# Performance work log

Hardware: AMD Instinct MI355X
Metric: run time of the kernel (lower is better)

The kernel has to match this reference:

```python
import jax, jax.numpy as jnp
import numpy as np

BATCH, SEQ, H, P, N, L = 8, 8192, 16, 64, 64, 64  # batch, seq, heads, d_head, d_state, block_len


def setup_inputs() -> dict:
    key = jax.random.key(0)
    k1, k2, k3 = jax.random.split(key, 3)
    X = jax.random.normal(k1, (BATCH, SEQ, H, P), dtype=jnp.float32)
    # A is the log-decay; scale down so exp(cumsum) stays finite over 8192 steps
    A = jax.random.normal(k2, (BATCH, SEQ, H), dtype=jnp.float32) * 0.02
    B = jax.random.normal(k3, (BATCH, SEQ, H, N), dtype=jnp.float32)
    return {"X": X, "A": A, "B": B}


def reference(X, A, B):
    b, s, h, p = X.shape
    n = B.shape[-1]
    l = L
    c = s // l  # n_chunks

    Xb = X.reshape(b, c, l, h, p)                      # (b,c,l,h,p)
    Ab = A.reshape(b, c, l, h).transpose(0, 3, 1, 2)   # (b,h,c,l)
    Bb = B.reshape(b, c, l, h, n)                      # (b,c,l,h,n)

    # intra-chunk cumulative decay
    A_cs = jnp.cumsum(Ab, axis=-1)                     # (b,h,c,l)
    decay_states = jnp.exp(A_cs[..., -1:] - A_cs)      # (b,h,c,l)

    # per-chunk state: sum_l decay * B outer X -> (b,c,h,p,n)
    states = jnp.einsum('bhcl,bclhn,bclhp->bchpn', decay_states, Bb, Xb)

    # prepend zero initial state
    init = jnp.zeros((b, 1, h, p, n), dtype=X.dtype)
    all_states = jnp.concatenate([init, states], axis=1)  # (b,c+1,h,p,n)

    # cross-chunk decay-weighted combination into final state
    A_ends = A_cs[..., -1]                                # (b,h,c)
    A_pad_cs = jnp.cumsum(jnp.pad(A_ends, ((0, 0), (0, 0), (1, 0))), axis=-1)  # (b,h,c+1)
    decay_chunk = jnp.exp(A_pad_cs[..., -1:] - A_pad_cs)  # (b,h,c+1)

    final_states = jnp.einsum('bhc,bchpn->bhpn', decay_chunk, all_states)  # (b,h,p,n)
    return final_states
```

## Files before the change

### kernel.cpp

```cpp
#include <hip/hip_runtime.h>

#define BATCH 8
#define SEQ   8192
#define NH    16
#define DP    64
#define ROWF  (NH*DP)
#define HGRP  4
#define NTHR  512
#define KT    32
#define RS    260

typedef __attribute__((ext_vector_type(8))) short bf16x8;
typedef __attribute__((ext_vector_type(4))) float f32x4;

static __device__ __forceinline__ unsigned pk2(float lo, float hi) {
    unsigned a = __builtin_bit_cast(unsigned, lo);
    unsigned b = __builtin_bit_cast(unsigned, hi);
    a = (a + 0x7FFFu + ((a >> 16) & 1u)) >> 16;
    b = (b + 0x7FFFu + ((b >> 16) & 1u)) & 0xFFFF0000u;
    return (a & 0xFFFFu) | b;
}

template<int NBLK>
__global__ __launch_bounds__(NTHR)
void k_partial(const float* __restrict__ Xg, const float* __restrict__ Ag,
               const float* __restrict__ Bg, float* __restrict__ part,
               float* __restrict__ blockA)
{
    constexpr int TB  = SEQ / NBLK;
    constexpr int Q   = TB / 64;
    constexpr int NKT = TB / KT;

    __shared__ unsigned XL[16][RS];
    __shared__ unsigned BL[16][RS];
    __shared__ float    WT[HGRP][TB];

    const int p    = blockIdx.x;
    const int xcd  = p & 7;
    const int q_   = p >> 3;
    const int hg   = q_ & 3;
    const int sidx = q_ >> 2;
    const int idx  = sidx * 8 + xcd;
    const int blk  = idx % NBLK;
    const int b    = idx / NBLK;

    const int tid  = threadIdx.x;
    const int w    = tid >> 6;
    const int lane = tid & 63;
    const int hloc = w >> 1;
    const int nh   = w & 1;
    const int h    = hg * HGRP + hloc;
    const int t0   = blk * TB;

    float c[Q];
    {
        const size_t abase = ((size_t)(b * SEQ + t0 + lane * Q)) * NH + h;
        float run = 0.f;
        #pragma unroll
        for (int k = 0; k < Q; ++k) { run += Ag[abase + (size_t)k * NH]; c[k] = run; }
    }
    float tsum = c[Q - 1], s = tsum;
    #pragma unroll
    for (int d = 1; d < 64; d <<= 1) {
        float o = __shfl_up(s, d, 64);
        if (lane >= d) s += o;
    }
    const float total = __shfl(s, 63, 64);
    const float excl  = s - tsum;
    if (nh == 0) {
        #pragma unroll
        for (int k = 0; k < Q; ++k)
            WT[hloc][lane * Q + k] = __expf(total - (excl + c[k]));
        if (lane == 63) blockA[(size_t)(b * NH + h) * NBLK + blk] = total;
    }

    f32x4 acc[4][2];
    #pragma unroll
    for (int mi = 0; mi < 4; ++mi)
        #pragma unroll
        for (int ni = 0; ni < 2; ++ni) acc[mi][ni] = (f32x4){0.f, 0.f, 0.f, 0.f};

    const int hl = lane >> 4;
    const int p4 = (lane & 15) * 4;
    const size_t gbase = (size_t)(b * SEQ + t0) * ROWF + hg * (HGRP * DP) + hl * DP + p4;

    auto issue = [&](int k, float4* lx, float4* lb) {
        if (k >= NKT) return;
        const size_t tb = gbase + (size_t)(k * KT + w * 4) * ROWF;
        #pragma unroll
        for (int i = 0; i < 4; ++i) {
            lx[i] = *(const float4*)(Xg + tb + (size_t)i * ROWF);
            lb[i] = *(const float4*)(Bg + tb + (size_t)i * ROWF);
        }
    };
    auto cwrite = [&](int k, const float4* lx, const float4* lb) {
        const int tIn = k * KT + w * 4;
        #pragma unroll
        for (int q2 = 0; q2 < 2; ++q2) {
            const float w0 = WT[hl][tIn + 2 * q2];
            const float w1 = WT[hl][tIn + 2 * q2 + 1];
            const int   tp = w * 2 + q2;
            const float* x0 = (const float*)&lx[2 * q2];
            const float* x1 = (const float*)&lx[2 * q2 + 1];
            const float* b0 = (const float*)&lb[2 * q2];
            const float* b1 = (const float*)&lb[2 * q2 + 1];
            uint4 xv, bv;
            xv.x = pk2(x0[0] * w0, x1[0] * w1);
            xv.y = pk2(x0[1] * w0, x1[1] * w1);
            xv.z = pk2(x0[2] * w0, x1[2] * w1);
            xv.w = pk2(x0[3] * w0, x1[3] * w1);
            bv.x = pk2(b0[0], b1[0]);
            bv.y = pk2(b0[1], b1[1]);
            bv.z = pk2(b0[2], b1[2]);
            bv.w = pk2(b0[3], b1[3]);
            *(uint4*)&XL[tp][hl * 64 + p4] = xv;
            *(uint4*)&BL[tp][hl * 64 + p4] = bv;
        }
    };
    auto compute = [&]() {
        const int r  = lane & 15;
        const int kg = lane >> 4;
        uint4 af[4], bf[2];
        #pragma unroll
        for (int mi = 0; mi < 4; ++mi) {
            const int row = hloc * 64 + mi * 16 + r;
            af[mi].x = XL[kg * 4 + 0][row];
            af[mi].y = XL[kg * 4 + 1][row];
            af[mi].z = XL[kg * 4 + 2][row];
            af[mi].w = XL[kg * 4 + 3][row];
        }
        #pragma unroll
        for (int ni = 0; ni < 2; ++ni) {
            const int row = hloc * 64 + nh * 32 + ni * 16 + r;
            bf[ni].x = BL[kg * 4 + 0][row];
            bf[ni].y = BL[kg * 4 + 1][row];
            bf[ni].z = BL[kg * 4 + 2][row];
            bf[ni].w = BL[kg * 4 + 3][row];
        }
        #pragma unroll
        for (int mi = 0; mi < 4; ++mi) {
            const bf16x8 a = __builtin_bit_cast(bf16x8, af[mi]);
            #pragma unroll
            for (int ni = 0; ni < 2; ++ni) {
                const bf16x8 bb = __builtin_bit_cast(bf16x8, bf[ni]);
                acc[mi][ni] = __builtin_amdgcn_mfma_f32_16x16x32_bf16(
                                  a, bb, acc[mi][ni], 0, 0, 0);
            }
        }
    };

    float4 sx0[4], sb0[4], sx1[4], sb1[4];
    issue(0, sx0, sb0);
    issue(1, sx1, sb1);
    __syncthreads();

    #pragma unroll 1
    for (int k = 0; k < NKT; k += 2) {
        cwrite(k, sx0, sb0);
        issue(k + 2, sx0, sb0);
        asm volatile("s_waitcnt lgkmcnt(0)" ::: "memory");
        __builtin_amdgcn_s_barrier();
        __builtin_amdgcn_sched_barrier(0);
        compute();
        __builtin_amdgcn_s_barrier();

        cwrite(k + 1, sx1, sb1);
        issue(k + 3, sx1, sb1);
        asm volatile("s_waitcnt lgkmcnt(0)" ::: "memory");
        __builtin_amdgcn_s_barrier();
        __builtin_amdgcn_sched_barrier(0);
        compute();
        __builtin_amdgcn_s_barrier();
    }

    float* dst = part + ((size_t)(b * NH + h) * NBLK + blk) * 4096;
    {
        const int r  = lane & 15;
        const int cg = lane >> 4;
        #pragma unroll
        for (int mi = 0; mi < 4; ++mi)
            #pragma unroll
            for (int ni = 0; ni < 2; ++ni)
                #pragma unroll
                for (int rr = 0; rr < 4; ++rr)
                    dst[(mi * 16 + cg * 4 + rr) * 64 + nh * 32 + ni * 16 + r] =
                        acc[mi][ni][rr];
    }
}

__global__ __launch_bounds__(256)
void k_combine(const float* __restrict__ part, const float* __restrict__ blockA,
               float* __restrict__ out, int nblk)
{
    const int idx = blockIdx.x * 256 + threadIdx.x;
    const int bh  = idx >> 12;
    const int e   = idx & 4095;
    float r = 0.f, run = 0.f;
    for (int q = nblk - 1; q >= 0; --q) {
        r   += __expf(run) * part[((size_t)bh * nblk + q) * 4096 + e];
        run += blockA[bh * nblk + q];
    }
    out[idx] = r;
}

extern "C" void kernel_launch(void* const* d_in, const int* in_sizes, int n_in,
                              void* d_out, int out_size, void* d_ws, size_t ws_size,
                              hipStream_t stream)
{
    const float* X = (const float*)d_in[0];
    const float* A = (const float*)d_in[1];
    const float* B = (const float*)d_in[2];
    float* out     = (float*)d_out;

    const size_t need32 = ((size_t)BATCH * NH * 32 * 4096 + (size_t)BATCH * NH * 32) * 4;
    const int nblk = (ws_size >= need32) ? 32 : 16;

    float* part   = (float*)d_ws;
    float* blockA = part + (size_t)BATCH * NH * nblk * 4096;

    if (nblk == 32)
        hipLaunchKernelGGL((k_partial<32>), dim3(BATCH * 4 * 32), dim3(NTHR), 0, stream,
                           X, A, B, part, blockA);
    else
        hipLaunchKernelGGL((k_partial<16>), dim3(BATCH * 4 * 16), dim3(NTHR), 0, stream,
                           X, A, B, part, blockA);

    hipLaunchKernelGGL(k_combine, dim3((BATCH * NH * 4096) / 256), dim3(256), 0, stream,
                       part, blockA, out, nblk);
}
```

Before: 135.7 us.

## Shrink head group to two heads per block and double grid size

Each workgroup now handles 2 heads with 256 threads instead of 4 heads with 512, and the grid doubles to 8 head-groups per batch/time-block. The global load mapping changes: each half-wave loads a 512-byte row segment covering two heads for alternating timesteps, and the LDS staging indices are remapped to match. This aims to raise occupancy and scheduling flexibility, at the cost of lower per-block reuse and the same LDS footprint per block (XL/BL arrays are still sized 260 wide though only 128 columns are used).

```diff
diff --git a/kernel.cpp b/kernel.cpp
--- a/kernel.cpp
+++ b/kernel.cpp
@@ -5,8 +5,8 @@
 #define NH    16
 #define DP    64
 #define ROWF  (NH*DP)
-#define HGRP  4
-#define NTHR  512
+#define HGRP  2
+#define NTHR  256
 #define KT    32
 #define RS    260
 
@@ -38,8 +38,8 @@
     const int p    = blockIdx.x;
     const int xcd  = p & 7;
     const int q_   = p >> 3;
-    const int hg   = q_ & 3;
-    const int sidx = q_ >> 2;
+    const int hgp  = q_ & 7;
+    const int sidx = q_ >> 3;
     const int idx  = sidx * 8 + xcd;
     const int blk  = idx % NBLK;
     const int b    = idx / NBLK;
@@ -49,7 +49,7 @@
     const int lane = tid & 63;
     const int hloc = w >> 1;
     const int nh   = w & 1;
-    const int h    = hg * HGRP + hloc;
+    const int h    = hgp * HGRP + hloc;
     const int t0   = blk * TB;
 
     float c[Q];
@@ -80,30 +80,31 @@
         #pragma unroll
         for (int ni = 0; ni < 2; ++ni) acc[mi][ni] = (f32x4){0.f, 0.f, 0.f, 0.f};
 
-    const int hl = lane >> 4;
-    const int p4 = (lane & 15) * 4;
-    const size_t gbase = (size_t)(b * SEQ + t0) * ROWF + hg * (HGRP * DP) + hl * DP + p4;
+    const int side = lane >> 5;
+    const int l32  = lane & 31;
+    const int hw   = l32 >> 4;
+    const size_t gbase = (size_t)(b * SEQ + t0) * ROWF + hgp * (HGRP * DP) + l32 * 4;
 
     auto issue = [&](int k, float4* lx, float4* lb) {
         if (k >= NKT) return;
-        const size_t tb = gbase + (size_t)(k * KT + w * 4) * ROWF;
+        const size_t tb = gbase + (size_t)(k * KT + w * 8 + side) * ROWF;
         #pragma unroll
         for (int i = 0; i < 4; ++i) {
-            lx[i] = *(const float4*)(Xg + tb + (size_t)i * ROWF);
-            lb[i] = *(const float4*)(Bg + tb + (size_t)i * ROWF);
+            lx[i] = *(const float4*)(Xg + tb + (size_t)(2 * i) * ROWF);
+            lb[i] = *(const float4*)(Bg + tb + (size_t)(2 * i) * ROWF);
         }
     };
     auto cwrite = [&](int k, const float4* lx, const float4* lb) {
-        const int tIn = k * KT + w * 4;
         #pragma unroll
         for (int q2 = 0; q2 < 2; ++q2) {
-            const float w0 = WT[hl][tIn + 2 * q2];
-            const float w1 = WT[hl][tIn + 2 * q2 + 1];
-            const int   tp = w * 2 + q2;
-            const float* x0 = (const float*)&lx[2 * q2];
-            const float* x1 = (const float*)&lx[2 * q2 + 1];
-            const float* b0 = (const float*)&lb[2 * q2];
-            const float* b1 = (const float*)&lb[2 * q2 + 1];
+            const int tlo = k * KT + w * 8 + 2 * q2 + side;
+            const float w0 = WT[hw][tlo];
+            const float w1 = WT[hw][tlo + 4];
+            const int   st = w * 4 + side * 2 + q2;
+            const float* x0 = (const float*)&lx[q2];
+            const float* x1 = (const float*)&lx[q2 + 2];
+            const float* b0 = (const float*)&lb[q2];
+            const float* b1 = (const float*)&lb[q2 + 2];
             uint4 xv, bv;
             xv.x = pk2(x0[0] * w0, x1[0] * w1);
             xv.y = pk2(x0[1] * w0, x1[1] * w1);
@@ -113,8 +114,8 @@
             bv.y = pk2(b0[1], b1[1]);
             bv.z = pk2(b0[2], b1[2]);
             bv.w = pk2(b0[3], b1[3]);
-            *(uint4*)&XL[tp][hl * 64 + p4] = xv;
-            *(uint4*)&BL[tp][hl * 64 + p4] = bv;
+            *(uint4*)&XL[st][l32 * 4] = xv;
+            *(uint4*)&BL[st][l32 * 4] = bv;
         }
     };
     auto compute = [&]() {
@@ -219,10 +220,10 @@
     float* blockA = part + (size_t)BATCH * NH * nblk * 4096;
 
     if (nblk == 32)
-        hipLaunchKernelGGL((k_partial<32>), dim3(BATCH * 4 * 32), dim3(NTHR), 0, stream,
+        hipLaunchKernelGGL((k_partial<32>), dim3(8 * BATCH * 32), dim3(NTHR), 0, stream,
                            X, A, B, part, blockA);
     else
-        hipLaunchKernelGGL((k_partial<16>), dim3(BATCH * 4 * 16), dim3(NTHR), 0, stream,
+        hipLaunchKernelGGL((k_partial<16>), dim3(8 * BATCH * 16), dim3(NTHR), 0, stream,
                            X, A, B, part, blockA);
 
     hipLaunchKernelGGL(k_combine, dim3((BATCH * NH * 4096) / 256), dim3(256), 0, stream,
```

Result: slower. 139.7 us (+2.9%).
